# Kernel optimization log

Hardware: AMD Instinct MI355X
Metric: run time of the kernel (lower is better)

The kernel has to match this reference:

```python
import jax, jax.numpy as jnp
import numpy as np

B, S, H = 128, 1024, 256
NEG = 1e9

def setup_inputs() -> dict:
    key = jax.random.key(0)
    ks = jax.random.split(key, 11)
    sc = 0.05
    return {
        'ref': jax.random.normal(ks[0], (B, S, H), jnp.float32),
        'query': jax.random.normal(ks[1], (B, H), jnp.float32),
        'mask': jax.random.randint(ks[2], (B, S), 0, 2, jnp.int32),
        'wg': jax.random.normal(ks[3], (H, H), jnp.float32) * sc,
        'bg': jax.random.normal(ks[4], (H,), jnp.float32) * sc,
        'wqg': jax.random.normal(ks[5], (H, H), jnp.float32) * sc,
        'vg': jax.random.normal(ks[6], (H,), jnp.float32) * sc,
        'wp': jax.random.normal(ks[7], (H, H), jnp.float32) * sc,
        'bp': jax.random.normal(ks[8], (H,), jnp.float32) * sc,
        'wqp': jax.random.normal(ks[9], (H, H), jnp.float32) * sc,
        'vp': jax.random.normal(ks[10], (H,), jnp.float32) * sc,
    }

def reference(ref, query, mask, wg, bg, wqg, vg, wp, bp, wqp, vp):
    # Bahdanau additive pointer attention with glimpse, per PointerDecoder.pointer_net
    maskf = mask.astype(ref.dtype)
    # glimpse attention
    enc_g = jnp.einsum('bsd,hd->bsh', ref, wg) + bg            # conv1d kernel=1
    q_g = jnp.einsum('bd,hd->bh', query, wqg)                   # w_q_g (no bias)
    scores_g = jnp.einsum('bsh,h->bs', jnp.tanh(enc_g + q_g[:, None, :]), vg)
    att_g = jax.nn.softmax(scores_g - maskf * NEG, axis=-1)     # [B,S]
    glimpse = jnp.einsum('bs,bsd->bd', att_g, ref) + query      # [B,H]
    # pointer scores
    enc_p = jnp.einsum('bsd,hd->bsh', ref, wp) + bp
    q_p = jnp.einsum('bd,hd->bh', glimpse, wqp)
    scores_p = jnp.einsum('bsh,h->bs', jnp.tanh(enc_p + q_p[:, None, :]), vp)
    masked_scores = scores_p - maskf * NEG                      # [B,S]
    return masked_scores
```

## Files before the change

### kernel.cpp

```cpp
#include <hip/hip_runtime.h>

#define Bb 128
#define Ss 1024
#define Hh 256
#define NEGF 1e9f

typedef short bf16x8 __attribute__((ext_vector_type(8)));
typedef float f32x4 __attribute__((ext_vector_type(4)));

__device__ __forceinline__ short f2bf(float f) {
    union { float f; unsigned u; } c; c.f = f;
    return (short)((c.u + 0x8000u) >> 16);
}

__device__ __forceinline__ float bfhi2f(unsigned u) {
    union { unsigned u; float f; } c; c.u = u & 0xFFFF0000u; return c.f;
}
__device__ __forceinline__ float bflo2f(unsigned u) {
    union { unsigned u; float f; } c; c.u = u << 16; return c.f;
}

__device__ __forceinline__ bf16x8 ld_bf8_f32(const float* p) {
    const float4* p4 = (const float4*)p;
    float4 a = p4[0], b = p4[1];
    bf16x8 r;
    r[0] = f2bf(a.x); r[1] = f2bf(a.y); r[2] = f2bf(a.z); r[3] = f2bf(a.w);
    r[4] = f2bf(b.x); r[5] = f2bf(b.y); r[6] = f2bf(b.z); r[7] = f2bf(b.w);
    return r;
}

__device__ __forceinline__ float fast_tanh(float x) {
    float cl = fminf(fmaxf(x, -10.f), 10.f);
    float e = __expf(2.f * cl);
    return __builtin_fmaf(-2.f, __builtin_amdgcn_rcpf(e + 1.f), 1.f);
}

__device__ __forceinline__ void stage16(const short* g, short* l) {
    __builtin_amdgcn_global_load_lds((const __attribute__((address_space(1))) void*)g,
                                     (__attribute__((address_space(3))) void*)l, 16, 0, 0);
}

__global__ __launch_bounds__(256) void prep_kernel(const float* __restrict__ wg,
                                                   const float* __restrict__ wp,
                                                   const float* __restrict__ query,
                                                   const float* __restrict__ wqg,
                                                   const float* __restrict__ bg,
                                                   short* __restrict__ wgb,
                                                   short* __restrict__ wpb,
                                                   float* __restrict__ qbias_g) {
    int blk = blockIdx.x, t = threadIdx.x;
    if (blk < 256) {
        int i = blk * 256 + t;
        wgb[i] = f2bf(wg[i]);
        wpb[i] = f2bf(wp[i]);
    } else {
        int b = blk - 256;
        const float4* qr = (const float4*)(query + b * Hh);
        const float4* wr = (const float4*)(wqg + t * Hh);
        float acc = 0.f;
#pragma unroll 8
        for (int i = 0; i < Hh / 4; ++i) {
            float4 q4 = qr[i], w4 = wr[i];
            acc += q4.x * w4.x + q4.y * w4.y + q4.z * w4.z + q4.w * w4.w;
        }
        qbias_g[b * Hh + t] = acc + bg[t];
    }
}

template <int MASKED, int LOADF32>
__global__ __launch_bounds__(256) void scores_mfma(const float* __restrict__ reff,
                                                   const short* __restrict__ refb_in,
                                                   short* __restrict__ refb_out,
                                                   const short* __restrict__ Wbf,
                                                   const float* __restrict__ qbias,
                                                   const float* __restrict__ vvec,
                                                   const int* __restrict__ mask,
                                                   float* __restrict__ out) {
    __shared__ short Wlds[2][4096];
    const int b = blockIdx.x;
    const int s0 = blockIdx.y * 64;
    const int t = threadIdx.x;
    const int wave = t >> 6;
    const int lane = t & 63;
    const int nl = lane & 15;
    const int quad = lane >> 4;
    const int rowbase = s0 + wave * 16;

    const int soff0 = (t & 15) * Hh + (t >> 6) * 32 + ((t >> 4) & 3) * 8;
    const int soff1 = soff0 + 128;
    const int dbase0 = wave * 512;
    const int dbase1 = 2048 + wave * 512;

    stage16(Wbf + soff0, &Wlds[0][dbase0]);
    stage16(Wbf + soff1, &Wlds[0][dbase1]);

    bf16x8 afrag[8];
    {
        const size_t rowoff = ((size_t)b * Ss + rowbase + nl) * Hh;
        if (LOADF32) {
            const float* rp = reff + rowoff;
#pragma unroll
            for (int kb = 0; kb < 8; ++kb)
                afrag[kb] = ld_bf8_f32(rp + kb * 32 + quad * 8);
            short* dst = refb_out + rowoff;
#pragma unroll
            for (int kb = 0; kb < 8; ++kb)
                *(bf16x8*)(dst + kb * 32 + quad * 8) = afrag[kb];
        } else {
            const short* rp = refb_in + rowoff;
#pragma unroll
            for (int kb = 0; kb < 8; ++kb)
                afrag[kb] = *(const bf16x8*)(rp + kb * 32 + quad * 8);
        }
    }
    __syncthreads();

    float sc[4] = {0.f, 0.f, 0.f, 0.f};

    for (int nc = 0; nc < 16; ++nc) {
        const int cur = nc & 1;
        if (nc < 15) {
            const short* g = Wbf + (size_t)(nc + 1) * 16 * Hh;
            stage16(g + soff0, &Wlds[1 - cur][dbase0]);
            stage16(g + soff1, &Wlds[1 - cur][dbase1]);
        }
        const int n = nc * 16 + nl;
        const float qb = qbias[b * Hh + n];
        const float vv = vvec[n];
        bf16x8 bfrag[8];
#pragma unroll
        for (int kb = 0; kb < 8; ++kb)
            bfrag[kb] = *(const bf16x8*)&Wlds[cur][kb * 512 + lane * 8];
        f32x4 c = {0.f, 0.f, 0.f, 0.f};
#pragma unroll
        for (int kb = 0; kb < 8; ++kb)
            c = __builtin_amdgcn_mfma_f32_16x16x32_bf16(afrag[kb], bfrag[kb], c, 0, 0, 0);
#pragma unroll
        for (int r = 0; r < 4; ++r)
            sc[r] += fast_tanh(c[r] + qb) * vv;
        __syncthreads();
    }

#pragma unroll
    for (int r = 0; r < 4; ++r) {
        float v = sc[r];
        v += __shfl_xor(v, 1, 64);
        v += __shfl_xor(v, 2, 64);
        v += __shfl_xor(v, 4, 64);
        v += __shfl_xor(v, 8, 64);
        sc[r] = v;
    }

    if (nl == 0) {
#pragma unroll
        for (int r = 0; r < 4; ++r) {
            int m = rowbase + quad * 4 + r;
            float v = sc[r];
            if (MASKED) v -= (float)mask[b * Ss + m] * NEGF;
            out[(size_t)b * Ss + m] = v;
        }
    }
}

__global__ __launch_bounds__(1024) void softmax_kernel(const float* __restrict__ scores,
                                                       const int* __restrict__ mask,
                                                       float* __restrict__ att) {
    int b = blockIdx.x, t = threadIdx.x;
    __shared__ float red[16];
    int idx = b * Ss + t;
    float x = scores[idx] - (float)mask[idx] * NEGF;

    float m = x;
#pragma unroll
    for (int o = 1; o < 64; o <<= 1) m = fmaxf(m, __shfl_xor(m, o, 64));
    if ((t & 63) == 0) red[t >> 6] = m;
    __syncthreads();
    float M = red[0];
#pragma unroll
    for (int j = 1; j < 16; ++j) M = fmaxf(M, red[j]);
    __syncthreads();

    float e = __expf(x - M);
    float s = e;
#pragma unroll
    for (int o = 1; o < 64; o <<= 1) s += __shfl_xor(s, o, 64);
    if ((t & 63) == 0) red[t >> 6] = s;
    __syncthreads();
    float S = 0.f;
#pragma unroll
    for (int j = 0; j < 16; ++j) S += red[j];

    att[idx] = e * __builtin_amdgcn_rcpf(S);
}

__global__ __launch_bounds__(256) void glimpse_part(const unsigned* __restrict__ refb,
                                                    const float* __restrict__ att,
                                                    float* __restrict__ gpart) {
    int b = blockIdx.x, q = blockIdx.y, t = threadIdx.x;
    const int c = t & 31;
    const int rg = t >> 5;
    __shared__ float part[8][Hh];
    const unsigned* base = refb + ((size_t)(b * Ss + q * 128)) * (Hh / 2);
    const float* ap = att + b * Ss + q * 128;

    float acc[8] = {0.f, 0.f, 0.f, 0.f, 0.f, 0.f, 0.f, 0.f};
#pragma unroll 4
    for (int it = 0; it < 16; ++it) {
        int row = it * 8 + rg;
        float a = ap[row];
        uint4 v = *(const uint4*)(base + (size_t)row * (Hh / 2) + c * 4);
        acc[0] += a * bflo2f(v.x); acc[1] += a * bfhi2f(v.x);
        acc[2] += a * bflo2f(v.y); acc[3] += a * bfhi2f(v.y);
        acc[4] += a * bflo2f(v.z); acc[5] += a * bfhi2f(v.z);
        acc[6] += a * bflo2f(v.w); acc[7] += a * bfhi2f(v.w);
    }
#pragma unroll
    for (int j = 0; j < 8; ++j) part[rg][c * 8 + j] = acc[j];
    __syncthreads();
    float s = 0.f;
#pragma unroll
    for (int g = 0; g < 8; ++g) s += part[g][t];
    gpart[(size_t)(b * 8 + q) * Hh + t] = s;
}

__global__ __launch_bounds__(256) void qbias_p_kernel(const float* __restrict__ gpart,
                                                      const float* __restrict__ query,
                                                      const float* __restrict__ wqp,
                                                      const float* __restrict__ bp,
                                                      float* __restrict__ out) {
    int b = blockIdx.x, t = threadIdx.x;
    __shared__ __align__(16) float gl[Hh];
    float g = query[b * Hh + t];
#pragma unroll
    for (int q = 0; q < 8; ++q) g += gpart[(b * 8 + q) * Hh + t];
    gl[t] = g;
    __syncthreads();
    const float4* wr = (const float4*)(wqp + t * Hh);
    const float4* gp = (const float4*)gl;
    float acc = 0.f;
#pragma unroll 8
    for (int i = 0; i < Hh / 4; ++i) {
        float4 w4 = wr[i];
        float4 g4 = gp[i];
        acc += w4.x * g4.x + w4.y * g4.y + w4.z * g4.z + w4.w * g4.w;
    }
    out[b * Hh + t] = acc + bp[t];
}

extern "C" void kernel_launch(void* const* d_in, const int* in_sizes, int n_in,
                              void* d_out, int out_size, void* d_ws, size_t ws_size,
                              hipStream_t stream) {
    const float* ref   = (const float*)d_in[0];
    const float* query = (const float*)d_in[1];
    const int*   mask  = (const int*)d_in[2];
    const float* wg    = (const float*)d_in[3];
    const float* bg    = (const float*)d_in[4];
    const float* wqg   = (const float*)d_in[5];
    const float* vg    = (const float*)d_in[6];
    const float* wp    = (const float*)d_in[7];
    const float* bp    = (const float*)d_in[8];
    const float* wqp   = (const float*)d_in[9];
    const float* vp    = (const float*)d_in[10];
    float* out = (float*)d_out;

    char* ws = (char*)d_ws;
    short* ref_bf   = (short*)(ws + 0);
    size_t off = (size_t)Bb * Ss * Hh * 2;
    short* wg_bf    = (short*)(ws + off);               off += 131072;
    short* wp_bf    = (short*)(ws + off);               off += 131072;
    float* qbias_g  = (float*)(ws + off);               off += 131072;
    float* qbias_p  = (float*)(ws + off);               off += 131072;
    float* scores_g = (float*)(ws + off);               off += 524288;
    float* att      = (float*)(ws + off);               off += 524288;
    float* gpart    = (float*)(ws + off);

    prep_kernel<<<384, 256, 0, stream>>>(wg, wp, query, wqg, bg, wg_bf, wp_bf, qbias_g);
    scores_mfma<0, 1><<<dim3(Bb, Ss / 64), 256, 0, stream>>>(
        ref, nullptr, ref_bf, wg_bf, qbias_g, vg, nullptr, scores_g);
    softmax_kernel<<<Bb, Ss, 0, stream>>>(scores_g, mask, att);
    glimpse_part<<<dim3(Bb, 8), 256, 0, stream>>>((const unsigned*)ref_bf, att, gpart);
    qbias_p_kernel<<<Bb, Hh, 0, stream>>>(gpart, query, wqp, bp, qbias_p);
    scores_mfma<1, 0><<<dim3(Bb, Ss / 64), 256, 0, stream>>>(
        nullptr, ref_bf, nullptr, wp_bf, qbias_p, vp, mask, out);
}
```

Before: 318.7 us.

## Make score kernels persistent with full weight matrix resident in LDS

Replaces the 2048-block scores kernel with 256 persistent blocks that each stage the whole 256x256 bf16 weight matrix (128 KB) into LDS once. Each wave then processes 128 rows in two passes of four 16-row tiles, reusing each LDS B-fragment across four MFMA tiles and removing per-chunk barriers and the redundant per-block weight staging. The cost is one block per CU, with 128 KB of dynamic shared memory and many more registers for four tiles of A fragments. That lowers occupancy and leaves less latency hiding for the global loads of ref.

```diff
diff --git a/kernel.cpp b/kernel.cpp
--- a/kernel.cpp
+++ b/kernel.cpp
@@ -68,96 +68,108 @@
 }
 
 template <int MASKED, int LOADF32>
-__global__ __launch_bounds__(256) void scores_mfma(const float* __restrict__ reff,
-                                                   const short* __restrict__ refb_in,
-                                                   short* __restrict__ refb_out,
-                                                   const short* __restrict__ Wbf,
-                                                   const float* __restrict__ qbias,
-                                                   const float* __restrict__ vvec,
-                                                   const int* __restrict__ mask,
-                                                   float* __restrict__ out) {
-    __shared__ short Wlds[2][4096];
-    const int b = blockIdx.x;
-    const int s0 = blockIdx.y * 64;
+__global__ __launch_bounds__(256, 1) void scores_persist(const float* __restrict__ reff,
+                                                         const short* __restrict__ refb_in,
+                                                         short* __restrict__ refb_out,
+                                                         const short* __restrict__ Wbf,
+                                                         const float* __restrict__ qbias,
+                                                         const float* __restrict__ vvec,
+                                                         const int* __restrict__ mask,
+                                                         float* __restrict__ out) {
+    extern __shared__ short Wlds[];
+    const int bk = blockIdx.x;
     const int t = threadIdx.x;
-    const int wave = t >> 6;
-    const int lane = t & 63;
-    const int nl = lane & 15;
-    const int quad = lane >> 4;
-    const int rowbase = s0 + wave * 16;
+    const int wave = t >> 6, lane = t & 63, nl = lane & 15, quad = lane >> 4;
+    const int b = bk >> 1;
+    const int srow0 = (bk & 1) * 512 + wave * 128;
 
     const int soff0 = (t & 15) * Hh + (t >> 6) * 32 + ((t >> 4) & 3) * 8;
     const int soff1 = soff0 + 128;
     const int dbase0 = wave * 512;
     const int dbase1 = 2048 + wave * 512;
 
-    stage16(Wbf + soff0, &Wlds[0][dbase0]);
-    stage16(Wbf + soff1, &Wlds[0][dbase1]);
-
-    bf16x8 afrag[8];
-    {
-        const size_t rowoff = ((size_t)b * Ss + rowbase + nl) * Hh;
-        if (LOADF32) {
-            const float* rp = reff + rowoff;
+#pragma unroll
+    for (int c = 0; c < 16; ++c) {
+        const short* g = Wbf + c * 16 * Hh;
+        stage16(g + soff0, &Wlds[c * 4096 + dbase0]);
+        stage16(g + soff1, &Wlds[c * 4096 + dbase1]);
+    }
+
+    float qb[16], vv[16];
+#pragma unroll
+    for (int nc = 0; nc < 16; ++nc) {
+        qb[nc] = qbias[b * Hh + nc * 16 + nl];
+        vv[nc] = vvec[nc * 16 + nl];
+    }
+    __syncthreads();
+
+    for (int pass = 0; pass < 2; ++pass) {
+        const int rowbase = srow0 + pass * 64;
+
+        bf16x8 af[4][8];
+#pragma unroll
+        for (int tile = 0; tile < 4; ++tile) {
+            const size_t rowoff = ((size_t)b * Ss + rowbase + tile * 16 + nl) * Hh;
+            if (LOADF32) {
+                const float* rp = reff + rowoff;
+#pragma unroll
+                for (int kb = 0; kb < 8; ++kb)
+                    af[tile][kb] = ld_bf8_f32(rp + kb * 32 + quad * 8);
+                short* dst = refb_out + rowoff;
+#pragma unroll
+                for (int kb = 0; kb < 8; ++kb)
+                    *(bf16x8*)(dst + kb * 32 + quad * 8) = af[tile][kb];
+            } else {
+                const short* rp = refb_in + rowoff;
+#pragma unroll
+                for (int kb = 0; kb < 8; ++kb)
+                    af[tile][kb] = *(const bf16x8*)(rp + kb * 32 + quad * 8);
+            }
+        }
+
+        float sc[4][4];
+#pragma unroll
+        for (int tile = 0; tile < 4; ++tile)
+#pragma unroll
+            for (int r = 0; r < 4; ++r) sc[tile][r] = 0.f;
+
+        for (int nc = 0; nc < 16; ++nc) {
+            bf16x8 bf[8];
 #pragma unroll
             for (int kb = 0; kb < 8; ++kb)
-                afrag[kb] = ld_bf8_f32(rp + kb * 32 + quad * 8);
-            short* dst = refb_out + rowoff;
-#pragma unroll
-            for (int kb = 0; kb < 8; ++kb)
-                *(bf16x8*)(dst + kb * 32 + quad * 8) = afrag[kb];
-        } else {
-            const short* rp = refb_in + rowoff;
-#pragma unroll
-            for (int kb = 0; kb < 8; ++kb)
-                afrag[kb] = *(const bf16x8*)(rp + kb * 32 + quad * 8);
-        }
-    }
-    __syncthreads();
-
-    float sc[4] = {0.f, 0.f, 0.f, 0.f};
-
-    for (int nc = 0; nc < 16; ++nc) {
-        const int cur = nc & 1;
-        if (nc < 15) {
-            const short* g = Wbf + (size_t)(nc + 1) * 16 * Hh;
-            stage16(g + soff0, &Wlds[1 - cur][dbase0]);
-            stage16(g + soff1, &Wlds[1 - cur][dbase1]);
-        }
-        const int n = nc * 16 + nl;
-        const float qb = qbias[b * Hh + n];
-        const float vv = vvec[n];
-        bf16x8 bfrag[8];
-#pragma unroll
-        for (int kb = 0; kb < 8; ++kb)
-            bfrag[kb] = *(const bf16x8*)&Wlds[cur][kb * 512 + lane * 8];
-        f32x4 c = {0.f, 0.f, 0.f, 0.f};
-#pragma unroll
-        for (int kb = 0; kb < 8; ++kb)
-            c = __builtin_amdgcn_mfma_f32_16x16x32_bf16(afrag[kb], bfrag[kb], c, 0, 0, 0);
-#pragma unroll
-        for (int r = 0; r < 4; ++r)
-            sc[r] += fast_tanh(c[r] + qb) * vv;
-        __syncthreads();
-    }
-
-#pragma unroll
-    for (int r = 0; r < 4; ++r) {
-        float v = sc[r];
-        v += __shfl_xor(v, 1, 64);
-        v += __shfl_xor(v, 2, 64);
-        v += __shfl_xor(v, 4, 64);
-        v += __shfl_xor(v, 8, 64);
-        sc[r] = v;
-    }
-
-    if (nl == 0) {
-#pragma unroll
-        for (int r = 0; r < 4; ++r) {
-            int m = rowbase + quad * 4 + r;
-            float v = sc[r];
-            if (MASKED) v -= (float)mask[b * Ss + m] * NEGF;
-            out[(size_t)b * Ss + m] = v;
+                bf[kb] = *(const bf16x8*)&Wlds[nc * 4096 + kb * 512 + lane * 8];
+#pragma unroll
+            for (int tile = 0; tile < 4; ++tile) {
+                f32x4 c = {0.f, 0.f, 0.f, 0.f};
+#pragma unroll
+                for (int kb = 0; kb < 8; ++kb)
+                    c = __builtin_amdgcn_mfma_f32_16x16x32_bf16(af[tile][kb], bf[kb], c, 0, 0, 0);
+#pragma unroll
+                for (int r = 0; r < 4; ++r)
+                    sc[tile][r] += fast_tanh(c[r] + qb[nc]) * vv[nc];
+            }
+        }
+
+#pragma unroll
+        for (int tile = 0; tile < 4; ++tile) {
+#pragma unroll
+            for (int r = 0; r < 4; ++r) {
+                float v = sc[tile][r];
+                v += __shfl_xor(v, 1, 64);
+                v += __shfl_xor(v, 2, 64);
+                v += __shfl_xor(v, 4, 64);
+                v += __shfl_xor(v, 8, 64);
+                sc[tile][r] = v;
+            }
+            if (nl == 0) {
+#pragma unroll
+                for (int r = 0; r < 4; ++r) {
+                    int m = rowbase + tile * 16 + quad * 4 + r;
+                    float v = sc[tile][r];
+                    if (MASKED) v -= (float)mask[b * Ss + m] * NEGF;
+                    out[(size_t)b * Ss + m] = v;
+                }
+            }
         }
     }
 }
@@ -275,11 +287,11 @@
     float* gpart    = (float*)(ws + off);
 
     prep_kernel<<<384, 256, 0, stream>>>(wg, wp, query, wqg, bg, wg_bf, wp_bf, qbias_g);
-    scores_mfma<0, 1><<<dim3(Bb, Ss / 64), 256, 0, stream>>>(
+    scores_persist<0, 1><<<256, 256, 131072, stream>>>(
         ref, nullptr, ref_bf, wg_bf, qbias_g, vg, nullptr, scores_g);
     softmax_kernel<<<Bb, Ss, 0, stream>>>(scores_g, mask, att);
     glimpse_part<<<dim3(Bb, 8), 256, 0, stream>>>((const unsigned*)ref_bf, att, gpart);
     qbias_p_kernel<<<Bb, Hh, 0, stream>>>(gpart, query, wqp, bp, qbias_p);
-    scores_mfma<1, 0><<<dim3(Bb, Ss / 64), 256, 0, stream>>>(
+    scores_persist<1, 0><<<256, 256, 131072, stream>>>(
         nullptr, ref_bf, nullptr, wp_bf, qbias_p, vp, mask, out);
 }
```

Measured after the change: 314.0 us. No clear change (-1.5%).
